# Performance work log

Hardware: AMD Instinct MI355X
Metric: run time of the kernel (lower is better)

## Reference

```python
import jax, jax.numpy as jnp
import numpy as np

B, V, FIN, H = 200, 40, 16, 128
NSW = 12          # switch edges
NE = 40           # regular edges
M = NE + NSW      # 52 total edges
MLP_HID = 1024
OUT = M + V + NSW # 104


def _build_graph():
    rng = np.random.default_rng(0)
    pairs = set()
    while len(pairs) < M:
        i, j = map(int, rng.integers(0, V, 2))
        if i < j:
            pairs.add((i, j))
    pairs = sorted(pairs)
    reg = np.array(pairs[:NE], np.int64)   # (NE,2)
    sw = np.array(pairs[NE:], np.int64)    # (NSW,2) row-major sorted, matches torch.nonzero order
    edges = np.concatenate([reg, sw], 0)   # switch edges last, matching graph_topo layout
    A = np.zeros((V, M), np.float32)
    A[edges[:, 0], np.arange(M)] = 1.0
    A[edges[:, 1], np.arange(M)] = -1.0
    return reg, sw, A


def setup_inputs():
    key = jax.random.key(0)
    ks = jax.random.split(key, 16)
    reg, sw, A = _build_graph()
    ei = jnp.broadcast_to(jnp.asarray(reg.T)[None], (B, 2, NE))
    si = jnp.broadcast_to(jnp.asarray(sw.T)[None], (B, 2, NSW))

    def w(k, shp, fan):
        return jax.random.normal(k, shp, jnp.float32) / np.sqrt(fan)

    return {
        'x_mod': jax.random.normal(ks[0], (B, V, FIN), jnp.float32),
        'ei': ei, 'si': si, 'A_inc': jnp.asarray(A),
        'embed': w(ks[1], (2, FIN), 1.0),
        'WU0': w(ks[2], (FIN, H), FIN), 'WV0': w(ks[3], (FIN, H), FIN),
        'WA0': w(ks[4], (FIN, H), FIN), 'WB0': w(ks[5], (FIN, H), FIN),
        'WC0': w(ks[6], (FIN, H), FIN),
        'WU1': w(ks[7], (H, H), H), 'WV1': w(ks[8], (H, H), H),
        'WA1': w(ks[9], (H, H), H), 'WB1': w(ks[10], (H, H), H),
        'WC1': w(ks[11], (H, H), H),
        'W1': w(ks[12], ((NSW + V) * H, MLP_HID), (NSW + V) * H),
        'b1': jnp.zeros((MLP_HID,), jnp.float32),
        'W2': w(ks[13], (MLP_HID, OUT), MLP_HID),
        'b2': jnp.zeros((OUT,), jnp.float32),
    }


def _layer(x, s, adj, smask, WU, WV, WA, WB, WC, residual):
    Ux = x @ WU
    Vx = x @ WV
    # gate features over dense VxV switch grid: e_ij = A s_ij + B x_i + C x_j
    e = jnp.einsum('bijf,fh->bijh', s, WA) + (x @ WB)[:, :, None, :] + (x @ WC)[:, None, :, :]
    gates = jax.nn.sigmoid(e) * smask[..., None]
    msg_edges = jnp.einsum('bij,bjh->bih', adj, Vx)   # regular-edge aggregation
    msg_sw = jnp.einsum('bijh,bjh->bih', gates, Vx)   # gated switch aggregation
    xh = jax.nn.relu(Ux + msg_edges + msg_sw)
    sh = jax.nn.relu(e)
    if residual:
        xh = x + xh
        sh = s + sh
    return xh, sh


def reference(x_mod, ei, si, A_inc, embed, WU0, WV0, WA0, WB0, WC0,
              WU1, WV1, WA1, WB1, WC1, W1, b1, W2, b2):
    i_sw, j_sw = si[0, 0], si[0, 1]   # switch indices (shared across batch)
    i_e, j_e = ei[0, 0], ei[0, 1]
    S = jnp.zeros((V, V), bool).at[i_sw, j_sw].set(True)   # upper-tri switch mask
    smask = jnp.broadcast_to(S, (B, V, V)).astype(x_mod.dtype)
    s0 = embed[S.astype(jnp.int32)]                        # (V,V,FIN) edge embedding
    s = jnp.broadcast_to(s0[None], (B, V, V, FIN))
    adj1 = jnp.zeros((V, V), x_mod.dtype).at[i_e, j_e].set(1.0)
    adj = jnp.broadcast_to((adj1 + adj1.T)[None], (B, V, V))
    x, s = _layer(x_mod, s, adj, smask, WU0, WV0, WA0, WB0, WC0, residual=False)
    x, s = _layer(x, s, adj, smask, WU1, WV1, WA1, WB1, WC1, residual=True)
    switches = s[:, i_sw, j_sw, :]                         # (B,NSW,H) irregular gather (torch.nonzero path)
    mlp_in = jnp.concatenate([switches.reshape(B, -1), x.reshape(B, -1)], axis=1)
    out = jax.nn.relu(mlp_in @ W1 + b1) @ W2 + b2          # (B,OUT)
    p_switch = jax.nn.sigmoid(out[:, -NSW:])
    graph_topo = jnp.ones((B, M), out.dtype).at[:, M - NSW:].set(p_switch)
    v = out[:, M:M + V].at[:, 0].set(1.0)
    p_fc = graph_topo * out[:, :M]
    q_fc = graph_topo * (v @ A_inc)                        # per-edge voltage difference flow
    pg = x_mod[:, :, 0] + jnp.einsum('vm,bm->bv', A_inc, p_fc)  # power balance completion
    qg = x_mod[:, :, 1] + jnp.einsum('vm,bm->bv', A_inc, q_fc)
    z = jnp.concatenate([p_fc, v, graph_topo], axis=1)     # (B, 2M+V)
    zc = jnp.concatenate([q_fc, pg, qg], axis=1)           # (B, M+2V)
    return z, zc
```

## Files before the change

### kernel.cpp

```cpp
#include <hip/hip_runtime.h>
#include <math.h>

#define B       200
#define V       40
#define FIN     16
#define H       128
#define NSW     12
#define NE      40
#define M       52
#define MLP_HID 1024
#define OUTD    104
#define MLP_IN  6656
#define ZDIM    144
#define ZCDIM   132
#define NCH     13
#define X1LD    136
#define MAXD    16

typedef __attribute__((ext_vector_type(8))) short bf16x8;
typedef __attribute__((ext_vector_type(4))) float f32x4;

__device__ __forceinline__ float sigmoidf(float x) {
    return 1.0f / (1.0f + expf(-x));
}
__device__ __forceinline__ unsigned short f2b(float x) {
    unsigned int u = __float_as_uint(x);
    u += 0x7fffu + ((u >> 16) & 1u);
    return (unsigned short)(u >> 16);
}
__device__ __forceinline__ float b2f(unsigned short s) {
    return __uint_as_float(((unsigned int)s) << 16);
}

__global__ __launch_bounds__(256) void k_prep(
        const float* __restrict__ WU0, const float* __restrict__ WV0,
        const float* __restrict__ WB0, const float* __restrict__ WC0,
        const float* __restrict__ WU1, const float* __restrict__ WV1,
        const float* __restrict__ WB1, const float* __restrict__ WC1,
        const float* __restrict__ WA1, const float* __restrict__ W2,
        unsigned short* __restrict__ W0t, unsigned short* __restrict__ Wt640,
        unsigned short* __restrict__ W2t) {
    int bx = blockIdx.x, tid = threadIdx.x;
    if (bx < 64) {
        int o0 = bx * 2048 + tid * 8;
#pragma unroll
        for (int i = 0; i < 8; ++i) {
            int o = o0 + i; int col = o >> 10, k = o & 1023;
            W2t[o] = (col < OUTD) ? f2b(W2[(size_t)k * OUTD + col]) : (unsigned short)0;
        }
    } else if (bx < 104) {
        int o0 = (bx - 64) * 2048 + tid * 8;
#pragma unroll
        for (int i = 0; i < 8; ++i) {
            int o = o0 + i; int col = o >> 7, f = o & 127;
            int m = col >> 7, hh = col & 127;
            const float* Ws = (m == 0) ? WU1 : (m == 1) ? WV1 : (m == 2) ? WB1
                            : (m == 3) ? WC1 : WA1;
            Wt640[o] = f2b(Ws[f * H + hh]);
        }
    } else {
        int o0 = (bx - 104) * 2048 + tid * 8;
#pragma unroll
        for (int i = 0; i < 8; ++i) {
            int o = o0 + i; int col = o >> 5, k = o & 31;
            int m = col >> 7, hh = col & 127;
            const float* Ws = (m == 0) ? WU0 : (m == 1) ? WV0 : (m == 2) ? WB0 : WC0;
            W0t[o] = (k < FIN) ? f2b(Ws[k * H + hh]) : (unsigned short)0;
        }
    }
}

__global__ __launch_bounds__(512) void k_gnn(const float* __restrict__ x,
        const int* __restrict__ ei, const int* __restrict__ si,
        const float* __restrict__ embed, const float* __restrict__ WA0,
        const unsigned short* __restrict__ W0t,
        const unsigned short* __restrict__ Wt640,
        unsigned short* __restrict__ Abf) {
    int b = blockIdx.x, tid = threadIdx.x;
    __shared__ unsigned short xb[48 * 40];
    __shared__ unsigned short uvbc[V * 512];
    __shared__ unsigned short x1l[64 * X1LD];
    __shared__ float gL[NSW * H];
    __shared__ float sA1l[NSW * H];
    __shared__ int   nbr[V][MAXD];
    __shared__ int   deg[V];

    int h = tid & 127, sub = tid >> 7;
    int lane = tid & 63, wv = tid >> 6;
    int lr = lane & 15, lk = lane >> 4;
    int n0w = wv * 64;

    for (int o = tid; o < 48 * 32; o += 512) {
        int r = o >> 5, k = o & 31;
        float v = (r < V && k < FIN) ? x[(size_t)b * V * FIN + r * FIN + k] : 0.f;
        xb[r * 40 + k] = f2b(v);
    }
    if (tid < V) deg[tid] = 0;
    for (int o = tid; o < 12 * 128; o += 512) {
        int rr = o >> 7;
        int row = (rr < 8) ? 40 + rr : 60 + (rr - 8);
        x1l[row * X1LD + (o & 127)] = 0;
    }
    __syncthreads();

    if (tid < NE) {
        int i = ei[tid], j = ei[NE + tid];
        int p = atomicAdd(&deg[i], 1); if (p < MAXD) nbr[i][p] = j;
        int q = atomicAdd(&deg[j], 1); if (q < MAXD) nbr[j][q] = i;
    } else if (tid < NE + NSW) {
        int k = tid - NE;
        int i = si[k], j = si[NSW + k];
        int p = atomicAdd(&deg[i], 1); if (p < MAXD) nbr[i][p] = j | ((k + 1) << 8);
    }
    {
        f32x4 acc[3][4];
#pragma unroll
        for (int rf = 0; rf < 3; ++rf)
#pragma unroll
            for (int cf = 0; cf < 4; ++cf) acc[rf][cf] = (f32x4){0.f, 0.f, 0.f, 0.f};
        int kseg = lk * 8;
        bf16x8 a0 = *(const bf16x8*)&xb[lr * 40 + kseg];
        bf16x8 a1 = *(const bf16x8*)&xb[(16 + lr) * 40 + kseg];
        bf16x8 a2 = *(const bf16x8*)&xb[(32 + lr) * 40 + kseg];
#pragma unroll
        for (int cf = 0; cf < 4; ++cf) {
            bf16x8 bf = *(const bf16x8*)&W0t[(n0w + cf * 16 + lr) * 32 + kseg];
            acc[0][cf] = __builtin_amdgcn_mfma_f32_16x16x32_bf16(a0, bf, acc[0][cf], 0, 0, 0);
            acc[1][cf] = __builtin_amdgcn_mfma_f32_16x16x32_bf16(a1, bf, acc[1][cf], 0, 0, 0);
            acc[2][cf] = __builtin_amdgcn_mfma_f32_16x16x32_bf16(a2, bf, acc[2][cf], 0, 0, 0);
        }
#pragma unroll
        for (int rf = 0; rf < 3; ++rf)
#pragma unroll
            for (int cf = 0; cf < 4; ++cf)
#pragma unroll
                for (int r = 0; r < 4; ++r) {
                    int row = rf * 16 + lk * 4 + r;
                    if (row < V) uvbc[row * 512 + n0w + cf * 16 + lr] = f2b(acc[rf][cf][r]);
                }
    }
    __syncthreads();

    {
        float sA0 = 0.f;
#pragma unroll
        for (int f = 0; f < FIN; ++f) sA0 += embed[FIN + f] * WA0[f * H + h];
        for (int k = sub; k < NSW; k += 4) {
            int i = si[k], j = si[NSW + k];
            float e0 = sA0 + b2f(uvbc[i * 512 + 256 + h]) + b2f(uvbc[j * 512 + 384 + h]);
            gL[k * H + h] = sigmoidf(e0);
            x1l[(48 + k) * X1LD + h] = f2b(fmaxf(e0, 0.f));
        }
    }
    __syncthreads();

    for (int i = sub * 10; i < sub * 10 + 10; ++i) {
        float acc = b2f(uvbc[i * 512 + h]);
        int d = deg[i]; if (d > MAXD) d = MAXD;
        for (int p = 0; p < d; ++p) {
            int ent = nbr[i][p];
            float vv = b2f(uvbc[(ent & 255) * 512 + 128 + h]);
            int g = ent >> 8;
            if (g) vv *= gL[(g - 1) * H + h];
            acc += vv;
        }
        x1l[i * X1LD + h] = f2b(fmaxf(acc, 0.f));
    }
    __syncthreads();

    {
        f32x4 acc[3][4], accs = (f32x4){0.f, 0.f, 0.f, 0.f};
#pragma unroll
        for (int rf = 0; rf < 3; ++rf)
#pragma unroll
            for (int cf = 0; cf < 4; ++cf) acc[rf][cf] = (f32x4){0.f, 0.f, 0.f, 0.f};
#pragma unroll
        for (int kk = 0; kk < 4; ++kk) {
            int kseg = kk * 32 + lk * 8;
            bf16x8 a0 = *(const bf16x8*)&x1l[lr * X1LD + kseg];
            bf16x8 a1 = *(const bf16x8*)&x1l[(16 + lr) * X1LD + kseg];
            bf16x8 a2 = *(const bf16x8*)&x1l[(32 + lr) * X1LD + kseg];
            bf16x8 as = *(const bf16x8*)&x1l[(48 + lr) * X1LD + kseg];
#pragma unroll
            for (int cf = 0; cf < 4; ++cf) {
                bf16x8 bf = *(const bf16x8*)&Wt640[(size_t)(n0w + cf * 16 + lr) * H + kseg];
                acc[0][cf] = __builtin_amdgcn_mfma_f32_16x16x32_bf16(a0, bf, acc[0][cf], 0, 0, 0);
                acc[1][cf] = __builtin_amdgcn_mfma_f32_16x16x32_bf16(a1, bf, acc[1][cf], 0, 0, 0);
                acc[2][cf] = __builtin_amdgcn_mfma_f32_16x16x32_bf16(a2, bf, acc[2][cf], 0, 0, 0);
            }
            bf16x8 bs = *(const bf16x8*)&Wt640[(size_t)(512 + wv * 16 + lr) * H + kseg];
            accs = __builtin_amdgcn_mfma_f32_16x16x32_bf16(as, bs, accs, 0, 0, 0);
        }
#pragma unroll
        for (int rf = 0; rf < 3; ++rf)
#pragma unroll
            for (int cf = 0; cf < 4; ++cf)
#pragma unroll
                for (int r = 0; r < 4; ++r) {
                    int row = rf * 16 + lk * 4 + r;
                    if (row < V) uvbc[row * 512 + n0w + cf * 16 + lr] = f2b(acc[rf][cf][r]);
                }
#pragma unroll
        for (int r = 0; r < 4; ++r) {
            int sr = lk * 4 + r;
            if (sr < NSW) sA1l[sr * H + wv * 16 + lr] = accs[r];
        }
    }
    __syncthreads();

    for (int k = sub; k < NSW; k += 4) {
        int i = si[k], j = si[NSW + k];
        float e1 = sA1l[k * H + h] + b2f(uvbc[i * 512 + 256 + h]) + b2f(uvbc[j * 512 + 384 + h]);
        gL[k * H + h] = sigmoidf(e1);
        float s1 = b2f(x1l[(48 + k) * X1LD + h]);
        Abf[(size_t)b * MLP_IN + k * H + h] = f2b(s1 + fmaxf(e1, 0.f));
    }
    __syncthreads();

    for (int i = sub * 10; i < sub * 10 + 10; ++i) {
        float acc = b2f(uvbc[i * 512 + h]);
        int d = deg[i]; if (d > MAXD) d = MAXD;
        for (int p = 0; p < d; ++p) {
            int ent = nbr[i][p];
            float vv = b2f(uvbc[(ent & 255) * 512 + 128 + h]);
            int g = ent >> 8;
            if (g) vv *= gL[(g - 1) * H + h];
            acc += vv;
        }
        float x2 = b2f(x1l[i * X1LD + h]) + fmaxf(acc, 0.f);
        Abf[(size_t)b * MLP_IN + NSW * H + i * H + h] = f2b(x2);
    }
}

__global__ __launch_bounds__(256) void k_mlp(const unsigned short* __restrict__ A,
        const float* __restrict__ W1, float* __restrict__ partial) {
    const int NK = 16;
    int tid = threadIdx.x;
    int lane = tid & 63, wvv = tid >> 6;
    int wr = (wvv >> 1) * 32, wc = (wvv & 1) * 32;
    int n0 = blockIdx.x * 64, m0 = blockIdx.y * 64;
    int kbase = blockIdx.z * NK * 32;

    __shared__ __align__(16) unsigned short a_lds[64 * 40];
    __shared__ __align__(16) unsigned short b_lds[64 * 40];

    f32x4 acc00 = {0,0,0,0}, acc01 = {0,0,0,0}, acc10 = {0,0,0,0}, acc11 = {0,0,0,0};

    int srow = tid >> 2, sseg = tid & 3;
    const int4* gA = (const int4*)(A + (size_t)(m0 + srow) * MLP_IN + kbase + sseg * 8);
    int lwsA = srow * 40 + sseg * 8;

    int bcol = tid & 63, bkg = tid >> 6;
    const float* gW = W1 + (size_t)(kbase + bkg * 8) * MLP_HID + n0 + bcol;
    int lwsB = bcol * 40 + bkg * 8;

    int a_off = (wr + (lane & 15)) * 40 + (lane >> 4) * 8;
    int b_off = (wc + (lane & 15)) * 40 + (lane >> 4) * 8;

    int4 ra = gA[0];
    float rfv[8];
#pragma unroll
    for (int i = 0; i < 8; ++i) rfv[i] = gW[(size_t)i * MLP_HID];

    for (int kk = 0; kk < NK; ++kk) {
        *(int4*)&a_lds[lwsA] = ra;
        union { unsigned short us[8]; int4 v; } pk;
#pragma unroll
        for (int i = 0; i < 8; ++i) pk.us[i] = f2b(rfv[i]);
        *(int4*)&b_lds[lwsB] = pk.v;
        __syncthreads();
        if (kk + 1 < NK) {
            ra = gA[(kk + 1) * 4];
            const float* g2 = gW + (size_t)(kk + 1) * 32 * MLP_HID;
#pragma unroll
            for (int i = 0; i < 8; ++i) rfv[i] = g2[(size_t)i * MLP_HID];
        }
        bf16x8 a0 = *(const bf16x8*)&a_lds[a_off];
        bf16x8 a1 = *(const bf16x8*)&a_lds[a_off + 16 * 40];
        bf16x8 b0 = *(const bf16x8*)&b_lds[b_off];
        bf16x8 b1 = *(const bf16x8*)&b_lds[b_off + 16 * 40];
        acc00 = __builtin_amdgcn_mfma_f32_16x16x32_bf16(a0, b0, acc00, 0, 0, 0);
        acc01 = __builtin_amdgcn_mfma_f32_16x16x32_bf16(a0, b1, acc01, 0, 0, 0);
        acc10 = __builtin_amdgcn_mfma_f32_16x16x32_bf16(a1, b0, acc10, 0, 0, 0);
        acc11 = __builtin_amdgcn_mfma_f32_16x16x32_bf16(a1, b1, acc11, 0, 0, 0);
        __syncthreads();
    }

    int crow = (lane >> 4) * 4, ccol = lane & 15;
    int row0 = m0 + wr + crow, row1 = row0 + 16;
    int col0 = n0 + wc + ccol, col1 = col0 + 16;
    float* dst = partial + (size_t)blockIdx.z * 256 * MLP_HID;
#pragma unroll
    for (int r = 0; r < 4; ++r) {
        dst[(size_t)(row0 + r) * MLP_HID + col0] = acc00[r];
        dst[(size_t)(row0 + r) * MLP_HID + col1] = acc01[r];
        dst[(size_t)(row1 + r) * MLP_HID + col0] = acc10[r];
        dst[(size_t)(row1 + r) * MLP_HID + col1] = acc11[r];
    }
}

template<int MODE>
__global__ __launch_bounds__(256) void k_gemm(const unsigned short* __restrict__ A,
        const unsigned short* __restrict__ Bt, void* __restrict__ Cout,
        int K, int nk, int ldc) {
    int tid = threadIdx.x;
    int lane = tid & 63, wv = tid >> 6;
    int wr = (wv >> 1) * 32, wc = (wv & 1) * 32;
    int n0 = blockIdx.x * 64, m0 = blockIdx.y * 64;
    size_t kbase = (size_t)blockIdx.z * nk * 32;

    __shared__ __align__(16) unsigned short a_lds[64 * 40];
    __shared__ __align__(16) unsigned short b_lds[64 * 40];

    f32x4 acc00 = {0,0,0,0}, acc01 = {0,0,0,0}, acc10 = {0,0,0,0}, acc11 = {0,0,0,0};

    int srow = tid >> 2, sseg = tid & 3;
    const int4* gA = (const int4*)(A + (size_t)(m0 + srow) * K + kbase + sseg * 8);
    const int4* gB = (const int4*)(Bt + (size_t)(n0 + srow) * K + kbase + sseg * 8);
    int lws = srow * 40 + sseg * 8;

    int a_off = (wr + (lane & 15)) * 40 + (lane >> 4) * 8;
    int b_off = (wc + (lane & 15)) * 40 + (lane >> 4) * 8;

    int4 ra = gA[0], rb = gB[0];
    for (int kk = 0; kk < nk; ++kk) {
        *(int4*)&a_lds[lws] = ra;
        *(int4*)&b_lds[lws] = rb;
        __syncthreads();
        if (kk + 1 < nk) { ra = gA[(kk + 1) * 4]; rb = gB[(kk + 1) * 4]; }
        bf16x8 a0 = *(const bf16x8*)&a_lds[a_off];
        bf16x8 a1 = *(const bf16x8*)&a_lds[a_off + 16 * 40];
        bf16x8 b0 = *(const bf16x8*)&b_lds[b_off];
        bf16x8 b1 = *(const bf16x8*)&b_lds[b_off + 16 * 40];
        acc00 = __builtin_amdgcn_mfma_f32_16x16x32_bf16(a0, b0, acc00, 0, 0, 0);
        acc01 = __builtin_amdgcn_mfma_f32_16x16x32_bf16(a0, b1, acc01, 0, 0, 0);
        acc10 = __builtin_amdgcn_mfma_f32_16x16x32_bf16(a1, b0, acc10, 0, 0, 0);
        acc11 = __builtin_amdgcn_mfma_f32_16x16x32_bf16(a1, b1, acc11, 0, 0, 0);
        __syncthreads();
    }

    int crow = (lane >> 4) * 4, ccol = lane & 15;
    int row0 = m0 + wr + crow, row1 = row0 + 16;
    int col0 = n0 + wc + ccol, col1 = col0 + 16;
    float* dst = (float*)Cout + (size_t)blockIdx.z * (gridDim.y * 64) * ldc;
#pragma unroll
    for (int r = 0; r < 4; ++r) {
        dst[(size_t)(row0 + r) * ldc + col0] = acc00[r];
        dst[(size_t)(row0 + r) * ldc + col1] = acc01[r];
        dst[(size_t)(row1 + r) * ldc + col0] = acc10[r];
        dst[(size_t)(row1 + r) * ldc + col1] = acc11[r];
    }
}

__global__ void k_mred(const float* __restrict__ partial, const float* __restrict__ b1,
                       unsigned short* __restrict__ hiddenb) {
    int i = blockIdx.x * 256 + threadIdx.x;
    float s = b1[i & (MLP_HID - 1)];
#pragma unroll
    for (int z = 0; z < NCH; ++z) s += partial[(size_t)z * 256 * MLP_HID + i];
    hiddenb[i] = f2b(fmaxf(s, 0.f));
}

__global__ __launch_bounds__(128) void k_fin(const float* __restrict__ partial2,
        const float* __restrict__ b2, const float* __restrict__ A,
        const float* __restrict__ x_mod, float* __restrict__ outp) {
    int b = blockIdx.x;
    int tid = threadIdx.x;
    __shared__ float o[OUTD];
    __shared__ float gt[M], vv[V], pfc[M], qfc[M];

    if (tid < OUTD) {
        float s = b2[tid];
#pragma unroll
        for (int z = 0; z < 4; ++z) s += partial2[(size_t)z * 256 * 128 + b * 128 + tid];
        o[tid] = s;
    }
    __syncthreads();

    if (tid < M) {
        float g = (tid < M - NSW) ? 1.0f : sigmoidf(o[M + V + (tid - (M - NSW))]);
        gt[tid] = g;
        pfc[tid] = g * o[tid];
    }
    if (tid < V) vv[tid] = (tid == 0) ? 1.0f : o[M + tid];
    __syncthreads();

    if (tid < M) {
        float acc = 0.f;
        for (int x = 0; x < V; ++x) acc += vv[x] * A[x * M + tid];
        qfc[tid] = gt[tid] * acc;
    }
    __syncthreads();

    float* zb = outp + (size_t)b * ZDIM;
    if (tid < M) zb[tid] = pfc[tid];
    if (tid < V) zb[M + tid] = vv[tid];
    if (tid < M) zb[M + V + tid] = gt[tid];

    float* zcb = outp + (size_t)B * ZDIM + (size_t)b * ZCDIM;
    if (tid < M) zcb[tid] = qfc[tid];
    if (tid < V) {
        float accp = 0.f, accq = 0.f;
        for (int m = 0; m < M; ++m) {
            float a = A[tid * M + m];
            accp += a * pfc[m];
            accq += a * qfc[m];
        }
        zcb[M + tid]     = x_mod[(size_t)(b * V + tid) * FIN + 0] + accp;
        zcb[M + V + tid] = x_mod[(size_t)(b * V + tid) * FIN + 1] + accq;
    }
}

extern "C" void kernel_launch(void* const* d_in, const int* in_sizes, int n_in,
                              void* d_out, int out_size, void* d_ws, size_t ws_size,
                              hipStream_t stream) {
    const float* x_mod = (const float*)d_in[0];
    const int*   ei    = (const int*)d_in[1];
    const int*   si    = (const int*)d_in[2];
    const float* A     = (const float*)d_in[3];
    const float* embed = (const float*)d_in[4];
    const float* WU0   = (const float*)d_in[5];
    const float* WV0   = (const float*)d_in[6];
    const float* WA0   = (const float*)d_in[7];
    const float* WB0   = (const float*)d_in[8];
    const float* WC0   = (const float*)d_in[9];
    const float* WU1   = (const float*)d_in[10];
    const float* WV1   = (const float*)d_in[11];
    const float* WA1   = (const float*)d_in[12];
    const float* WB1   = (const float*)d_in[13];
    const float* WC1   = (const float*)d_in[14];
    const float* W1    = (const float*)d_in[15];
    const float* b1    = (const float*)d_in[16];
    const float* W2    = (const float*)d_in[17];
    const float* b2    = (const float*)d_in[18];
    float* out = (float*)d_out;

    char* ws = (char*)d_ws;
    unsigned short* W0t      = (unsigned short*)(ws + 0);
    unsigned short* Wt640    = (unsigned short*)(ws + 32768);
    unsigned short* W2t      = (unsigned short*)(ws + 196608);
    unsigned short* Abf      = (unsigned short*)(ws + 458752);
    float*          partialM = (float*)(ws + 3866624);
    unsigned short* hiddenb  = (unsigned short*)(ws + 17498112);
    float*          partial2 = (float*)(ws + 18022400);

    k_prep<<<112, 256, 0, stream>>>(WU0, WV0, WB0, WC0, WU1, WV1, WB1, WC1, WA1, W2,
                                    W0t, Wt640, W2t);
    k_gnn<<<B, 512, 0, stream>>>(x_mod, ei, si, embed, WA0, W0t, Wt640, Abf);
    k_mlp<<<dim3(16, 4, NCH), 256, 0, stream>>>(Abf, W1, partialM);
    k_mred<<<256 * MLP_HID / 256, 256, 0, stream>>>(partialM, b1, hiddenb);
    k_gemm<2><<<dim3(2, 4, 4), 256, 0, stream>>>(hiddenb, W2t, partial2, MLP_HID, 8, 128);
    k_fin<<<B, 128, 0, stream>>>(partial2, b2, A, x_mod, out);
}
```

Measured before the change: 56.48 us.

## Fuse all stages into one cooperative persistent kernel with grid syncs

Replaces six separate kernel launches (weight prep, GNN, MLP split-K, reduction, second GEMM, finalize) with a single cooperative kernel of 256 blocks. Stages are separated by grid-wide syncs and share one LDS union. The aim is to remove per-launch overhead and inter-kernel gaps. In exchange, the stages now run at a fixed grid size with larger blocks, grid.sync has its own cost, and occupancy is constrained by the cooperative launch.

```diff
diff --git a/kernel.cpp b/kernel.cpp
--- a/kernel.cpp
+++ b/kernel.cpp
@@ -1,5 +1,8 @@
 #include <hip/hip_runtime.h>
+#include <hip/hip_cooperative_groups.h>
 #include <math.h>
+
+namespace cg = cooperative_groups;
 
 #define B       200
 #define V       40
@@ -32,382 +35,401 @@
     return __uint_as_float(((unsigned int)s) << 16);
 }
 
-__global__ __launch_bounds__(256) void k_prep(
+__global__ __launch_bounds__(512, 2) void k_all(
+        const float* __restrict__ x_mod, const int* __restrict__ ei,
+        const int* __restrict__ si, const float* __restrict__ Ainc,
+        const float* __restrict__ embed,
         const float* __restrict__ WU0, const float* __restrict__ WV0,
-        const float* __restrict__ WB0, const float* __restrict__ WC0,
+        const float* __restrict__ WA0, const float* __restrict__ WB0,
+        const float* __restrict__ WC0,
         const float* __restrict__ WU1, const float* __restrict__ WV1,
-        const float* __restrict__ WB1, const float* __restrict__ WC1,
-        const float* __restrict__ WA1, const float* __restrict__ W2,
+        const float* __restrict__ WA1, const float* __restrict__ WB1,
+        const float* __restrict__ WC1,
+        const float* __restrict__ W1, const float* __restrict__ b1,
+        const float* __restrict__ W2, const float* __restrict__ b2,
         unsigned short* __restrict__ W0t, unsigned short* __restrict__ Wt640,
-        unsigned short* __restrict__ W2t) {
-    int bx = blockIdx.x, tid = threadIdx.x;
-    if (bx < 64) {
-        int o0 = bx * 2048 + tid * 8;
-#pragma unroll
-        for (int i = 0; i < 8; ++i) {
-            int o = o0 + i; int col = o >> 10, k = o & 1023;
+        unsigned short* __restrict__ W2t, unsigned short* __restrict__ Abf,
+        float* __restrict__ partialM, unsigned short* __restrict__ hiddenb,
+        float* __restrict__ partial2, float* __restrict__ outp) {
+    cg::grid_group grid = cg::this_grid();
+    int bid = blockIdx.x, tid = threadIdx.x;
+    int gtid = bid * 512 + tid;
+
+    __shared__ union {
+        struct {
+            unsigned short xb[48 * 40];
+            unsigned short uvbc[V * 512];
+            unsigned short x1l[64 * X1LD];
+            float gL[NSW * H];
+            float sA1l[NSW * H];
+            int   nbr[V][MAXD];
+            int   deg[V];
+        } g;
+        struct { unsigned short a[64 * 40]; unsigned short b[128 * 40]; } m;
+        struct { float o[OUTD]; float gt[M]; float vv[V]; float pfc[M]; float qfc[M]; } f;
+    } lds;
+
+    for (int t = gtid; t < 16384 + 81920 + 131072; t += 131072) {
+        if (t < 16384) {
+            int col = t >> 5, k = t & 31;
+            int mm = col >> 7, hh = col & 127;
+            const float* Ws = (mm == 0) ? WU0 : (mm == 1) ? WV0 : (mm == 2) ? WB0 : WC0;
+            W0t[t] = (k < FIN) ? f2b(Ws[k * H + hh]) : (unsigned short)0;
+        } else if (t < 16384 + 81920) {
+            int o = t - 16384;
+            int col = o >> 7, ff = o & 127;
+            int mm = col >> 7, hh = col & 127;
+            const float* Ws = (mm == 0) ? WU1 : (mm == 1) ? WV1 : (mm == 2) ? WB1
+                            : (mm == 3) ? WC1 : WA1;
+            Wt640[o] = f2b(Ws[ff * H + hh]);
+        } else {
+            int o = t - (16384 + 81920);
+            int col = o >> 10, k = o & 1023;
             W2t[o] = (col < OUTD) ? f2b(W2[(size_t)k * OUTD + col]) : (unsigned short)0;
         }
-    } else if (bx < 104) {
-        int o0 = (bx - 64) * 2048 + tid * 8;
-#pragma unroll
-        for (int i = 0; i < 8; ++i) {
-            int o = o0 + i; int col = o >> 7, f = o & 127;
-            int m = col >> 7, hh = col & 127;
-            const float* Ws = (m == 0) ? WU1 : (m == 1) ? WV1 : (m == 2) ? WB1
-                            : (m == 3) ? WC1 : WA1;
-            Wt640[o] = f2b(Ws[f * H + hh]);
-        }
-    } else {
-        int o0 = (bx - 104) * 2048 + tid * 8;
-#pragma unroll
-        for (int i = 0; i < 8; ++i) {
-            int o = o0 + i; int col = o >> 5, k = o & 31;
-            int m = col >> 7, hh = col & 127;
-            const float* Ws = (m == 0) ? WU0 : (m == 1) ? WV0 : (m == 2) ? WB0 : WC0;
-            W0t[o] = (k < FIN) ? f2b(Ws[k * H + hh]) : (unsigned short)0;
-        }
-    }
-}
-
-__global__ __launch_bounds__(512) void k_gnn(const float* __restrict__ x,
-        const int* __restrict__ ei, const int* __restrict__ si,
-        const float* __restrict__ embed, const float* __restrict__ WA0,
-        const unsigned short* __restrict__ W0t,
-        const unsigned short* __restrict__ Wt640,
-        unsigned short* __restrict__ Abf) {
-    int b = blockIdx.x, tid = threadIdx.x;
-    __shared__ unsigned short xb[48 * 40];
-    __shared__ unsigned short uvbc[V * 512];
-    __shared__ unsigned short x1l[64 * X1LD];
-    __shared__ float gL[NSW * H];
-    __shared__ float sA1l[NSW * H];
-    __shared__ int   nbr[V][MAXD];
-    __shared__ int   deg[V];
-
-    int h = tid & 127, sub = tid >> 7;
-    int lane = tid & 63, wv = tid >> 6;
-    int lr = lane & 15, lk = lane >> 4;
-    int n0w = wv * 64;
-
-    for (int o = tid; o < 48 * 32; o += 512) {
-        int r = o >> 5, k = o & 31;
-        float v = (r < V && k < FIN) ? x[(size_t)b * V * FIN + r * FIN + k] : 0.f;
-        xb[r * 40 + k] = f2b(v);
-    }
-    if (tid < V) deg[tid] = 0;
-    for (int o = tid; o < 12 * 128; o += 512) {
-        int rr = o >> 7;
-        int row = (rr < 8) ? 40 + rr : 60 + (rr - 8);
-        x1l[row * X1LD + (o & 127)] = 0;
-    }
-    __syncthreads();
-
-    if (tid < NE) {
-        int i = ei[tid], j = ei[NE + tid];
-        int p = atomicAdd(&deg[i], 1); if (p < MAXD) nbr[i][p] = j;
-        int q = atomicAdd(&deg[j], 1); if (q < MAXD) nbr[j][q] = i;
-    } else if (tid < NE + NSW) {
-        int k = tid - NE;
-        int i = si[k], j = si[NSW + k];
-        int p = atomicAdd(&deg[i], 1); if (p < MAXD) nbr[i][p] = j | ((k + 1) << 8);
-    }
-    {
-        f32x4 acc[3][4];
-#pragma unroll
-        for (int rf = 0; rf < 3; ++rf)
-#pragma unroll
-            for (int cf = 0; cf < 4; ++cf) acc[rf][cf] = (f32x4){0.f, 0.f, 0.f, 0.f};
-        int kseg = lk * 8;
-        bf16x8 a0 = *(const bf16x8*)&xb[lr * 40 + kseg];
-        bf16x8 a1 = *(const bf16x8*)&xb[(16 + lr) * 40 + kseg];
-        bf16x8 a2 = *(const bf16x8*)&xb[(32 + lr) * 40 + kseg];
-#pragma unroll
-        for (int cf = 0; cf < 4; ++cf) {
-            bf16x8 bf = *(const bf16x8*)&W0t[(n0w + cf * 16 + lr) * 32 + kseg];
-            acc[0][cf] = __builtin_amdgcn_mfma_f32_16x16x32_bf16(a0, bf, acc[0][cf], 0, 0, 0);
-            acc[1][cf] = __builtin_amdgcn_mfma_f32_16x16x32_bf16(a1, bf, acc[1][cf], 0, 0, 0);
-            acc[2][cf] = __builtin_amdgcn_mfma_f32_16x16x32_bf16(a2, bf, acc[2][cf], 0, 0, 0);
-        }
-#pragma unroll
-        for (int rf = 0; rf < 3; ++rf)
-#pragma unroll
-            for (int cf = 0; cf < 4; ++cf)
-#pragma unroll
-                for (int r = 0; r < 4; ++r) {
-                    int row = rf * 16 + lk * 4 + r;
-                    if (row < V) uvbc[row * 512 + n0w + cf * 16 + lr] = f2b(acc[rf][cf][r]);
-                }
-    }
-    __syncthreads();
-
-    {
-        float sA0 = 0.f;
-#pragma unroll
-        for (int f = 0; f < FIN; ++f) sA0 += embed[FIN + f] * WA0[f * H + h];
-        for (int k = sub; k < NSW; k += 4) {
+    }
+    grid.sync();
+
+    if (bid < B) {
+        int b = bid;
+        unsigned short* xb   = lds.g.xb;
+        unsigned short* uvbc = lds.g.uvbc;
+        unsigned short* x1l  = lds.g.x1l;
+        float* gL   = lds.g.gL;
+        float* sA1l = lds.g.sA1l;
+        int (*nbr)[MAXD] = lds.g.nbr;
+        int* deg = lds.g.deg;
+
+        int h = tid & 127, sub = tid >> 7;
+        int lane = tid & 63, wv = tid >> 6;
+        int lr = lane & 15, lk = lane >> 4;
+        int n0w = wv * 64;
+
+        for (int o = tid; o < 48 * 32; o += 512) {
+            int r = o >> 5, k = o & 31;
+            float v = (r < V && k < FIN) ? x_mod[(size_t)b * V * FIN + r * FIN + k] : 0.f;
+            xb[r * 40 + k] = f2b(v);
+        }
+        if (tid < V) deg[tid] = 0;
+        for (int o = tid; o < 12 * 128; o += 512) {
+            int rr = o >> 7;
+            int row = (rr < 8) ? 40 + rr : 60 + (rr - 8);
+            x1l[row * X1LD + (o & 127)] = 0;
+        }
+        __syncthreads();
+
+        if (tid < NE) {
+            int i = ei[tid], j = ei[NE + tid];
+            int p = atomicAdd(&deg[i], 1); if (p < MAXD) nbr[i][p] = j;
+            int q = atomicAdd(&deg[j], 1); if (q < MAXD) nbr[j][q] = i;
+        } else if (tid < NE + NSW) {
+            int k = tid - NE;
             int i = si[k], j = si[NSW + k];
-            float e0 = sA0 + b2f(uvbc[i * 512 + 256 + h]) + b2f(uvbc[j * 512 + 384 + h]);
-            gL[k * H + h] = sigmoidf(e0);
-            x1l[(48 + k) * X1LD + h] = f2b(fmaxf(e0, 0.f));
-        }
-    }
-    __syncthreads();
-
-    for (int i = sub * 10; i < sub * 10 + 10; ++i) {
-        float acc = b2f(uvbc[i * 512 + h]);
-        int d = deg[i]; if (d > MAXD) d = MAXD;
-        for (int p = 0; p < d; ++p) {
-            int ent = nbr[i][p];
-            float vv = b2f(uvbc[(ent & 255) * 512 + 128 + h]);
-            int g = ent >> 8;
-            if (g) vv *= gL[(g - 1) * H + h];
-            acc += vv;
-        }
-        x1l[i * X1LD + h] = f2b(fmaxf(acc, 0.f));
-    }
-    __syncthreads();
-
-    {
-        f32x4 acc[3][4], accs = (f32x4){0.f, 0.f, 0.f, 0.f};
-#pragma unroll
-        for (int rf = 0; rf < 3; ++rf)
-#pragma unroll
-            for (int cf = 0; cf < 4; ++cf) acc[rf][cf] = (f32x4){0.f, 0.f, 0.f, 0.f};
-#pragma unroll
-        for (int kk = 0; kk < 4; ++kk) {
-            int kseg = kk * 32 + lk * 8;
-            bf16x8 a0 = *(const bf16x8*)&x1l[lr * X1LD + kseg];
-            bf16x8 a1 = *(const bf16x8*)&x1l[(16 + lr) * X1LD + kseg];
-            bf16x8 a2 = *(const bf16x8*)&x1l[(32 + lr) * X1LD + kseg];
-            bf16x8 as = *(const bf16x8*)&x1l[(48 + lr) * X1LD + kseg];
+            int p = atomicAdd(&deg[i], 1); if (p < MAXD) nbr[i][p] = j | ((k + 1) << 8);
+        }
+        {
+            f32x4 acc[3][4];
+#pragma unroll
+            for (int rf = 0; rf < 3; ++rf)
+#pragma unroll
+                for (int cf = 0; cf < 4; ++cf) acc[rf][cf] = (f32x4){0.f, 0.f, 0.f, 0.f};
+            int kseg = lk * 8;
+            bf16x8 a0 = *(const bf16x8*)&xb[lr * 40 + kseg];
+            bf16x8 a1 = *(const bf16x8*)&xb[(16 + lr) * 40 + kseg];
+            bf16x8 a2 = *(const bf16x8*)&xb[(32 + lr) * 40 + kseg];
 #pragma unroll
             for (int cf = 0; cf < 4; ++cf) {
-                bf16x8 bf = *(const bf16x8*)&Wt640[(size_t)(n0w + cf * 16 + lr) * H + kseg];
+                bf16x8 bf = *(const bf16x8*)&W0t[(n0w + cf * 16 + lr) * 32 + kseg];
                 acc[0][cf] = __builtin_amdgcn_mfma_f32_16x16x32_bf16(a0, bf, acc[0][cf], 0, 0, 0);
                 acc[1][cf] = __builtin_amdgcn_mfma_f32_16x16x32_bf16(a1, bf, acc[1][cf], 0, 0, 0);
                 acc[2][cf] = __builtin_amdgcn_mfma_f32_16x16x32_bf16(a2, bf, acc[2][cf], 0, 0, 0);
             }
-            bf16x8 bs = *(const bf16x8*)&Wt640[(size_t)(512 + wv * 16 + lr) * H + kseg];
-            accs = __builtin_amdgcn_mfma_f32_16x16x32_bf16(as, bs, accs, 0, 0, 0);
-        }
-#pragma unroll
-        for (int rf = 0; rf < 3; ++rf)
-#pragma unroll
-            for (int cf = 0; cf < 4; ++cf)
+#pragma unroll
+            for (int rf = 0; rf < 3; ++rf)
+#pragma unroll
+                for (int cf = 0; cf < 4; ++cf)
+#pragma unroll
+                    for (int r = 0; r < 4; ++r) {
+                        int row = rf * 16 + lk * 4 + r;
+                        if (row < V) uvbc[row * 512 + n0w + cf * 16 + lr] = f2b(acc[rf][cf][r]);
+                    }
+        }
+        __syncthreads();
+
+        {
+            float sA0 = 0.f;
+#pragma unroll
+            for (int f = 0; f < FIN; ++f) sA0 += embed[FIN + f] * WA0[f * H + h];
+            for (int k = sub; k < NSW; k += 4) {
+                int i = si[k], j = si[NSW + k];
+                float e0 = sA0 + b2f(uvbc[i * 512 + 256 + h]) + b2f(uvbc[j * 512 + 384 + h]);
+                gL[k * H + h] = sigmoidf(e0);
+                x1l[(48 + k) * X1LD + h] = f2b(fmaxf(e0, 0.f));
+            }
+        }
+        __syncthreads();
+
+        for (int i = sub * 10; i < sub * 10 + 10; ++i) {
+            float acc = b2f(uvbc[i * 512 + h]);
+            int d = deg[i]; if (d > MAXD) d = MAXD;
+            for (int p = 0; p < d; ++p) {
+                int ent = nbr[i][p];
+                float vv = b2f(uvbc[(ent & 255) * 512 + 128 + h]);
+                int g = ent >> 8;
+                if (g) vv *= gL[(g - 1) * H + h];
+                acc += vv;
+            }
+            x1l[i * X1LD + h] = f2b(fmaxf(acc, 0.f));
+        }
+        __syncthreads();
+
+        {
+            f32x4 acc[3][4], accs = (f32x4){0.f, 0.f, 0.f, 0.f};
+#pragma unroll
+            for (int rf = 0; rf < 3; ++rf)
+#pragma unroll
+                for (int cf = 0; cf < 4; ++cf) acc[rf][cf] = (f32x4){0.f, 0.f, 0.f, 0.f};
+#pragma unroll
+            for (int kk = 0; kk < 4; ++kk) {
+                int kseg = kk * 32 + lk * 8;
+                bf16x8 a0 = *(const bf16x8*)&x1l[lr * X1LD + kseg];
+                bf16x8 a1 = *(const bf16x8*)&x1l[(16 + lr) * X1LD + kseg];
+                bf16x8 a2 = *(const bf16x8*)&x1l[(32 + lr) * X1LD + kseg];
+                bf16x8 as = *(const bf16x8*)&x1l[(48 + lr) * X1LD + kseg];
+#pragma unroll
+                for (int cf = 0; cf < 4; ++cf) {
+                    bf16x8 bf = *(const bf16x8*)&Wt640[(size_t)(n0w + cf * 16 + lr) * H + kseg];
+                    acc[0][cf] = __builtin_amdgcn_mfma_f32_16x16x32_bf16(a0, bf, acc[0][cf], 0, 0, 0);
+                    acc[1][cf] = __builtin_amdgcn_mfma_f32_16x16x32_bf16(a1, bf, acc[1][cf], 0, 0, 0);
+                    acc[2][cf] = __builtin_amdgcn_mfma_f32_16x16x32_bf16(a2, bf, acc[2][cf], 0, 0, 0);
+                }
+                bf16x8 bs = *(const bf16x8*)&Wt640[(size_t)(512 + wv * 16 + lr) * H + kseg];
+                accs = __builtin_amdgcn_mfma_f32_16x16x32_bf16(as, bs, accs, 0, 0, 0);
+            }
+#pragma unroll
+            for (int rf = 0; rf < 3; ++rf)
+#pragma unroll
+                for (int cf = 0; cf < 4; ++cf)
+#pragma unroll
+                    for (int r = 0; r < 4; ++r) {
+                        int row = rf * 16 + lk * 4 + r;
+                        if (row < V) uvbc[row * 512 + n0w + cf * 16 + lr] = f2b(acc[rf][cf][r]);
+                    }
+#pragma unroll
+            for (int r = 0; r < 4; ++r) {
+                int sr = lk * 4 + r;
+                if (sr < NSW) sA1l[sr * H + wv * 16 + lr] = accs[r];
+            }
+        }
+        __syncthreads();
+
+        for (int k = sub; k < NSW; k += 4) {
+            int i = si[k], j = si[NSW + k];
+            float e1 = sA1l[k * H + h] + b2f(uvbc[i * 512 + 256 + h]) + b2f(uvbc[j * 512 + 384 + h]);
+            gL[k * H + h] = sigmoidf(e1);
+            float s1 = b2f(x1l[(48 + k) * X1LD + h]);
+            Abf[(size_t)b * MLP_IN + k * H + h] = f2b(s1 + fmaxf(e1, 0.f));
+        }
+        __syncthreads();
+
+        for (int i = sub * 10; i < sub * 10 + 10; ++i) {
+            float acc = b2f(uvbc[i * 512 + h]);
+            int d = deg[i]; if (d > MAXD) d = MAXD;
+            for (int p = 0; p < d; ++p) {
+                int ent = nbr[i][p];
+                float vv = b2f(uvbc[(ent & 255) * 512 + 128 + h]);
+                int g = ent >> 8;
+                if (g) vv *= gL[(g - 1) * H + h];
+                acc += vv;
+            }
+            float x2 = b2f(x1l[i * X1LD + h]) + fmaxf(acc, 0.f);
+            Abf[(size_t)b * MLP_IN + NSW * H + i * H + h] = f2b(x2);
+        }
+    }
+    grid.sync();
+
+    {
+        unsigned short* a_lds = lds.m.a;
+        unsigned short* b_lds = lds.m.b;
+        int lane = tid & 63, wv = tid >> 6;
+        int lr = lane & 15, lk = lane >> 4;
+        int wr = (wv >> 2) * 32, wc = (wv & 3) * 32;
+
+        for (int it = 0; it < 2; ++it) {
+            int j = bid + it * 256;
+            bool valid = (j < 416);
+            int jj = valid ? j : 0;
+            int z = jj >> 5;
+            int rem = jj & 31;
+            int n0 = (rem & 7) << 7;
+            int m0 = (rem >> 3) << 6;
+            int kbase = z << 9;
+
+            int srow = tid >> 3, sseg = tid & 7;
+            const unsigned short* gA = Abf + (size_t)(m0 + srow) * MLP_IN + kbase + sseg * 4;
+            int lwsA = srow * 40 + sseg * 4;
+            int bcol = tid & 127, bkg = tid >> 7;
+            const float* gW = W1 + (size_t)(kbase + bkg * 8) * MLP_HID + n0 + bcol;
+            int lwsB = bcol * 40 + bkg * 8;
+            int a_off = (wr + lr) * 40 + lk * 8;
+            int b_off = (wc + lr) * 40 + lk * 8;
+
+            f32x4 acc00 = {0,0,0,0}, acc01 = {0,0,0,0}, acc10 = {0,0,0,0}, acc11 = {0,0,0,0};
+            int2 ra = *(const int2*)gA;
+            float rfv[8];
+#pragma unroll
+            for (int i = 0; i < 8; ++i) rfv[i] = gW[(size_t)i * MLP_HID];
+
+            for (int kk = 0; kk < 16; ++kk) {
+                *(int2*)&a_lds[lwsA] = ra;
+                union { unsigned short us[8]; int4 v; } pk;
+#pragma unroll
+                for (int i = 0; i < 8; ++i) pk.us[i] = f2b(rfv[i]);
+                *(int4*)&b_lds[lwsB] = pk.v;
+                __syncthreads();
+                if (kk + 1 < 16) {
+                    ra = *(const int2*)(gA + (kk + 1) * 32);
+                    const float* g2 = gW + (size_t)(kk + 1) * 32 * MLP_HID;
+#pragma unroll
+                    for (int i = 0; i < 8; ++i) rfv[i] = g2[(size_t)i * MLP_HID];
+                }
+                bf16x8 a0 = *(const bf16x8*)&a_lds[a_off];
+                bf16x8 a1 = *(const bf16x8*)&a_lds[a_off + 16 * 40];
+                bf16x8 b0 = *(const bf16x8*)&b_lds[b_off];
+                bf16x8 b1 = *(const bf16x8*)&b_lds[b_off + 16 * 40];
+                acc00 = __builtin_amdgcn_mfma_f32_16x16x32_bf16(a0, b0, acc00, 0, 0, 0);
+                acc01 = __builtin_amdgcn_mfma_f32_16x16x32_bf16(a0, b1, acc01, 0, 0, 0);
+                acc10 = __builtin_amdgcn_mfma_f32_16x16x32_bf16(a1, b0, acc10, 0, 0, 0);
+                acc11 = __builtin_amdgcn_mfma_f32_16x16x32_bf16(a1, b1, acc11, 0, 0, 0);
+                __syncthreads();
+            }
+            if (valid) {
+                int crow = lk * 4, ccol = lr;
+                int row0 = m0 + wr + crow, row1 = row0 + 16;
+                int col0 = n0 + wc + ccol, col1 = col0 + 16;
+                float* dst = partialM + (size_t)z * 256 * MLP_HID;
 #pragma unroll
                 for (int r = 0; r < 4; ++r) {
-                    int row = rf * 16 + lk * 4 + r;
-                    if (row < V) uvbc[row * 512 + n0w + cf * 16 + lr] = f2b(acc[rf][cf][r]);
+                    dst[(size_t)(row0 + r) * MLP_HID + col0] = acc00[r];
+                    dst[(size_t)(row0 + r) * MLP_HID + col1] = acc01[r];
+                    dst[(size_t)(row1 + r) * MLP_HID + col0] = acc10[r];
+                    dst[(size_t)(row1 + r) * MLP_HID + col1] = acc11[r];
                 }
+            }
+        }
+    }
+    grid.sync();
+
+    for (int t = gtid; t < 256 * MLP_HID; t += 131072) {
+        float s = b1[t & (MLP_HID - 1)];
+#pragma unroll
+        for (int z = 0; z < NCH; ++z) s += partialM[(size_t)z * 256 * MLP_HID + t];
+        hiddenb[t] = f2b(fmaxf(s, 0.f));
+    }
+    grid.sync();
+
+    if (bid < 16) {
+        unsigned short* a_lds = lds.m.a;
+        unsigned short* b_lds = lds.m.b;
+        int m0 = (bid >> 2) * 64;
+        int z = bid & 3;
+        int kbase = z * 256;
+        int lane = tid & 63, wv = tid >> 6;
+        int lr = lane & 15, lk = lane >> 4;
+        int wr = (wv >> 2) * 32, wc = (wv & 3) * 32;
+
+        int srow = tid >> 3, sseg = tid & 7;
+        const unsigned short* gA = hiddenb + (size_t)(m0 + srow) * MLP_HID + kbase + sseg * 4;
+        int lwsA = srow * 40 + sseg * 4;
+        int brow = tid >> 2, bseg = tid & 3;
+        const unsigned short* gB = W2t + (size_t)brow * MLP_HID + kbase + bseg * 8;
+        int lwsB = brow * 40 + bseg * 8;
+        int a_off = (wr + lr) * 40 + lk * 8;
+        int b_off = (wc + lr) * 40 + lk * 8;
+
+        f32x4 acc00 = {0,0,0,0}, acc01 = {0,0,0,0}, acc10 = {0,0,0,0}, acc11 = {0,0,0,0};
+        int2 ra = *(const int2*)gA;
+        int4 rb = *(const int4*)gB;
+        for (int kk = 0; kk < 8; ++kk) {
+            *(int2*)&a_lds[lwsA] = ra;
+            *(int4*)&b_lds[lwsB] = rb;
+            __syncthreads();
+            if (kk + 1 < 8) {
+                ra = *(const int2*)(gA + (kk + 1) * 32);
+                rb = *(const int4*)(gB + (kk + 1) * 32);
+            }
+            bf16x8 a0 = *(const bf16x8*)&a_lds[a_off];
+            bf16x8 a1 = *(const bf16x8*)&a_lds[a_off + 16 * 40];
+            bf16x8 b0 = *(const bf16x8*)&b_lds[b_off];
+            bf16x8 b1 = *(const bf16x8*)&b_lds[b_off + 16 * 40];
+            acc00 = __builtin_amdgcn_mfma_f32_16x16x32_bf16(a0, b0, acc00, 0, 0, 0);
+            acc01 = __builtin_amdgcn_mfma_f32_16x16x32_bf16(a0, b1, acc01, 0, 0, 0);
+            acc10 = __builtin_amdgcn_mfma_f32_16x16x32_bf16(a1, b0, acc10, 0, 0, 0);
+            acc11 = __builtin_amdgcn_mfma_f32_16x16x32_bf16(a1, b1, acc11, 0, 0, 0);
+            __syncthreads();
+        }
+        int crow = lk * 4, ccol = lr;
+        int row0 = m0 + wr + crow, row1 = row0 + 16;
+        int col0 = wc + ccol, col1 = col0 + 16;
+        float* dst = partial2 + (size_t)z * 256 * 128;
 #pragma unroll
         for (int r = 0; r < 4; ++r) {
-            int sr = lk * 4 + r;
-            if (sr < NSW) sA1l[sr * H + wv * 16 + lr] = accs[r];
-        }
-    }
-    __syncthreads();
-
-    for (int k = sub; k < NSW; k += 4) {
-        int i = si[k], j = si[NSW + k];
-        float e1 = sA1l[k * H + h] + b2f(uvbc[i * 512 + 256 + h]) + b2f(uvbc[j * 512 + 384 + h]);
-        gL[k * H + h] = sigmoidf(e1);
-        float s1 = b2f(x1l[(48 + k) * X1LD + h]);
-        Abf[(size_t)b * MLP_IN + k * H + h] = f2b(s1 + fmaxf(e1, 0.f));
-    }
-    __syncthreads();
-
-    for (int i = sub * 10; i < sub * 10 + 10; ++i) {
-        float acc = b2f(uvbc[i * 512 + h]);
-        int d = deg[i]; if (d > MAXD) d = MAXD;
-        for (int p = 0; p < d; ++p) {
-            int ent = nbr[i][p];
-            float vv = b2f(uvbc[(ent & 255) * 512 + 128 + h]);
-            int g = ent >> 8;
-            if (g) vv *= gL[(g - 1) * H + h];
-            acc += vv;
-        }
-        float x2 = b2f(x1l[i * X1LD + h]) + fmaxf(acc, 0.f);
-        Abf[(size_t)b * MLP_IN + NSW * H + i * H + h] = f2b(x2);
-    }
-}
-
-__global__ __launch_bounds__(256) void k_mlp(const unsigned short* __restrict__ A,
-        const float* __restrict__ W1, float* __restrict__ partial) {
-    const int NK = 16;
-    int tid = threadIdx.x;
-    int lane = tid & 63, wvv = tid >> 6;
-    int wr = (wvv >> 1) * 32, wc = (wvv & 1) * 32;
-    int n0 = blockIdx.x * 64, m0 = blockIdx.y * 64;
-    int kbase = blockIdx.z * NK * 32;
-
-    __shared__ __align__(16) unsigned short a_lds[64 * 40];
-    __shared__ __align__(16) unsigned short b_lds[64 * 40];
-
-    f32x4 acc00 = {0,0,0,0}, acc01 = {0,0,0,0}, acc10 = {0,0,0,0}, acc11 = {0,0,0,0};
-
-    int srow = tid >> 2, sseg = tid & 3;
-    const int4* gA = (const int4*)(A + (size_t)(m0 + srow) * MLP_IN + kbase + sseg * 8);
-    int lwsA = srow * 40 + sseg * 8;
-
-    int bcol = tid & 63, bkg = tid >> 6;
-    const float* gW = W1 + (size_t)(kbase + bkg * 8) * MLP_HID + n0 + bcol;
-    int lwsB = bcol * 40 + bkg * 8;
-
-    int a_off = (wr + (lane & 15)) * 40 + (lane >> 4) * 8;
-    int b_off = (wc + (lane & 15)) * 40 + (lane >> 4) * 8;
-
-    int4 ra = gA[0];
-    float rfv[8];
-#pragma unroll
-    for (int i = 0; i < 8; ++i) rfv[i] = gW[(size_t)i * MLP_HID];
-
-    for (int kk = 0; kk < NK; ++kk) {
-        *(int4*)&a_lds[lwsA] = ra;
-        union { unsigned short us[8]; int4 v; } pk;
-#pragma unroll
-        for (int i = 0; i < 8; ++i) pk.us[i] = f2b(rfv[i]);
-        *(int4*)&b_lds[lwsB] = pk.v;
-        __syncthreads();
-        if (kk + 1 < NK) {
-            ra = gA[(kk + 1) * 4];
-            const float* g2 = gW + (size_t)(kk + 1) * 32 * MLP_HID;
-#pragma unroll
-            for (int i = 0; i < 8; ++i) rfv[i] = g2[(size_t)i * MLP_HID];
-        }
-        bf16x8 a0 = *(const bf16x8*)&a_lds[a_off];
-        bf16x8 a1 = *(const bf16x8*)&a_lds[a_off + 16 * 40];
-        bf16x8 b0 = *(const bf16x8*)&b_lds[b_off];
-        bf16x8 b1 = *(const bf16x8*)&b_lds[b_off + 16 * 40];
-        acc00 = __builtin_amdgcn_mfma_f32_16x16x32_bf16(a0, b0, acc00, 0, 0, 0);
-        acc01 = __builtin_amdgcn_mfma_f32_16x16x32_bf16(a0, b1, acc01, 0, 0, 0);
-        acc10 = __builtin_amdgcn_mfma_f32_16x16x32_bf16(a1, b0, acc10, 0, 0, 0);
-        acc11 = __builtin_amdgcn_mfma_f32_16x16x32_bf16(a1, b1, acc11, 0, 0, 0);
-        __syncthreads();
-    }
-
-    int crow = (lane >> 4) * 4, ccol = lane & 15;
-    int row0 = m0 + wr + crow, row1 = row0 + 16;
-    int col0 = n0 + wc + ccol, col1 = col0 + 16;
-    float* dst = partial + (size_t)blockIdx.z * 256 * MLP_HID;
-#pragma unroll
-    for (int r = 0; r < 4; ++r) {
-        dst[(size_t)(row0 + r) * MLP_HID + col0] = acc00[r];
-        dst[(size_t)(row0 + r) * MLP_HID + col1] = acc01[r];
-        dst[(size_t)(row1 + r) * MLP_HID + col0] = acc10[r];
-        dst[(size_t)(row1 + r) * MLP_HID + col1] = acc11[r];
-    }
-}
-
-template<int MODE>
-__global__ __launch_bounds__(256) void k_gemm(const unsigned short* __restrict__ A,
-        const unsigned short* __restrict__ Bt, void* __restrict__ Cout,
-        int K, int nk, int ldc) {
-    int tid = threadIdx.x;
-    int lane = tid & 63, wv = tid >> 6;
-    int wr = (wv >> 1) * 32, wc = (wv & 1) * 32;
-    int n0 = blockIdx.x * 64, m0 = blockIdx.y * 64;
-    size_t kbase = (size_t)blockIdx.z * nk * 32;
-
-    __shared__ __align__(16) unsigned short a_lds[64 * 40];
-    __shared__ __align__(16) unsigned short b_lds[64 * 40];
-
-    f32x4 acc00 = {0,0,0,0}, acc01 = {0,0,0,0}, acc10 = {0,0,0,0}, acc11 = {0,0,0,0};
-
-    int srow = tid >> 2, sseg = tid & 3;
-    const int4* gA = (const int4*)(A + (size_t)(m0 + srow) * K + kbase + sseg * 8);
-    const int4* gB = (const int4*)(Bt + (size_t)(n0 + srow) * K + kbase + sseg * 8);
-    int lws = srow * 40 + sseg * 8;
-
-    int a_off = (wr + (lane & 15)) * 40 + (lane >> 4) * 8;
-    int b_off = (wc + (lane & 15)) * 40 + (lane >> 4) * 8;
-
-    int4 ra = gA[0], rb = gB[0];
-    for (int kk = 0; kk < nk; ++kk) {
-        *(int4*)&a_lds[lws] = ra;
-        *(int4*)&b_lds[lws] = rb;
-        __syncthreads();
-        if (kk + 1 < nk) { ra = gA[(kk + 1) * 4]; rb = gB[(kk + 1) * 4]; }
-        bf16x8 a0 = *(const bf16x8*)&a_lds[a_off];
-        bf16x8 a1 = *(const bf16x8*)&a_lds[a_off + 16 * 40];
-        bf16x8 b0 = *(const bf16x8*)&b_lds[b_off];
-        bf16x8 b1 = *(const bf16x8*)&b_lds[b_off + 16 * 40];
-        acc00 = __builtin_amdgcn_mfma_f32_16x16x32_bf16(a0, b0, acc00, 0, 0, 0);
-        acc01 = __builtin_amdgcn_mfma_f32_16x16x32_bf16(a0, b1, acc01, 0, 0, 0);
-        acc10 = __builtin_amdgcn_mfma_f32_16x16x32_bf16(a1, b0, acc10, 0, 0, 0);
-        acc11 = __builtin_amdgcn_mfma_f32_16x16x32_bf16(a1, b1, acc11, 0, 0, 0);
-        __syncthreads();
-    }
-
-    int crow = (lane >> 4) * 4, ccol = lane & 15;
-    int row0 = m0 + wr + crow, row1 = row0 + 16;
-    int col0 = n0 + wc + ccol, col1 = col0 + 16;
-    float* dst = (float*)Cout + (size_t)blockIdx.z * (gridDim.y * 64) * ldc;
-#pragma unroll
-    for (int r = 0; r < 4; ++r) {
-        dst[(size_t)(row0 + r) * ldc + col0] = acc00[r];
-        dst[(size_t)(row0 + r) * ldc + col1] = acc01[r];
-        dst[(size_t)(row1 + r) * ldc + col0] = acc10[r];
-        dst[(size_t)(row1 + r) * ldc + col1] = acc11[r];
-    }
-}
-
-__global__ void k_mred(const float* __restrict__ partial, const float* __restrict__ b1,
-                       unsigned short* __restrict__ hiddenb) {
-    int i = blockIdx.x * 256 + threadIdx.x;
-    float s = b1[i & (MLP_HID - 1)];
-#pragma unroll
-    for (int z = 0; z < NCH; ++z) s += partial[(size_t)z * 256 * MLP_HID + i];
-    hiddenb[i] = f2b(fmaxf(s, 0.f));
-}
-
-__global__ __launch_bounds__(128) void k_fin(const float* __restrict__ partial2,
-        const float* __restrict__ b2, const float* __restrict__ A,
-        const float* __restrict__ x_mod, float* __restrict__ outp) {
-    int b = blockIdx.x;
-    int tid = threadIdx.x;
-    __shared__ float o[OUTD];
-    __shared__ float gt[M], vv[V], pfc[M], qfc[M];
-
-    if (tid < OUTD) {
-        float s = b2[tid];
-#pragma unroll
-        for (int z = 0; z < 4; ++z) s += partial2[(size_t)z * 256 * 128 + b * 128 + tid];
-        o[tid] = s;
-    }
-    __syncthreads();
-
-    if (tid < M) {
-        float g = (tid < M - NSW) ? 1.0f : sigmoidf(o[M + V + (tid - (M - NSW))]);
-        gt[tid] = g;
-        pfc[tid] = g * o[tid];
-    }
-    if (tid < V) vv[tid] = (tid == 0) ? 1.0f : o[M + tid];
-    __syncthreads();
-
-    if (tid < M) {
-        float acc = 0.f;
-        for (int x = 0; x < V; ++x) acc += vv[x] * A[x * M + tid];
-        qfc[tid] = gt[tid] * acc;
-    }
-    __syncthreads();
-
-    float* zb = outp + (size_t)b * ZDIM;
-    if (tid < M) zb[tid] = pfc[tid];
-    if (tid < V) zb[M + tid] = vv[tid];
-    if (tid < M) zb[M + V + tid] = gt[tid];
-
-    float* zcb = outp + (size_t)B * ZDIM + (size_t)b * ZCDIM;
-    if (tid < M) zcb[tid] = qfc[tid];
-    if (tid < V) {
-        float accp = 0.f, accq = 0.f;
-        for (int m = 0; m < M; ++m) {
-            float a = A[tid * M + m];
-            accp += a * pfc[m];
-            accq += a * qfc[m];
-        }
-        zcb[M + tid]     = x_mod[(size_t)(b * V + tid) * FIN + 0] + accp;
-        zcb[M + V + tid] = x_mod[(size_t)(b * V + tid) * FIN + 1] + accq;
+            dst[(size_t)(row0 + r) * 128 + col0] = acc00[r];
+            dst[(size_t)(row0 + r) * 128 + col1] = acc01[r];
+            dst[(size_t)(row1 + r) * 128 + col0] = acc10[r];
+            dst[(size_t)(row1 + r) * 128 + col1] = acc11[r];
+        }
+    }
+    grid.sync();
+
+    if (bid < B) {
+        int b = bid;
+        float* o   = lds.f.o;
+        float* gt  = lds.f.gt;
+        float* vv  = lds.f.vv;
+        float* pfc = lds.f.pfc;
+        float* qfc = lds.f.qfc;
+
+        if (tid < OUTD) {
+            float s = b2[tid];
+#pragma unroll
+            for (int z = 0; z < 4; ++z) s += partial2[(size_t)z * 256 * 128 + b * 128 + tid];
+            o[tid] = s;
+        }
+        __syncthreads();
+
+        if (tid < M) {
+            float g = (tid < M - NSW) ? 1.0f : sigmoidf(o[M + V + (tid - (M - NSW))]);
+            gt[tid] = g;
+            pfc[tid] = g * o[tid];
+        }
+        if (tid < V) vv[tid] = (tid == 0) ? 1.0f : o[M + tid];
+        __syncthreads();
+
+        if (tid < M) {
+            float acc = 0.f;
+            for (int xx = 0; xx < V; ++xx) acc += vv[xx] * Ainc[xx * M + tid];
+            qfc[tid] = gt[tid] * acc;
+        }
+        __syncthreads();
+
+        float* zb = outp + (size_t)b * ZDIM;
+        if (tid < M) zb[tid] = pfc[tid];
+        if (tid < V) zb[M + tid] = vv[tid];
+        if (tid < M) zb[M + V + tid] = gt[tid];
+
+        float* zcb = outp + (size_t)B * ZDIM + (size_t)b * ZCDIM;
+        if (tid < M) zcb[tid] = qfc[tid];
+        if (tid < V) {
+            float accp = 0.f, accq = 0.f;
+            for (int mm = 0; mm < M; ++mm) {
+                float a = Ainc[tid * M + mm];
+                accp += a * pfc[mm];
+                accq += a * qfc[mm];
+            }
+            zcb[M + tid]     = x_mod[(size_t)(b * V + tid) * FIN + 0] + accp;
+            zcb[M + V + tid] = x_mod[(size_t)(b * V + tid) * FIN + 1] + accq;
+        }
     }
 }
 
@@ -417,7 +439,7 @@
     const float* x_mod = (const float*)d_in[0];
     const int*   ei    = (const int*)d_in[1];
     const int*   si    = (const int*)d_in[2];
-    const float* A     = (const float*)d_in[3];
+    const float* Ainc  = (const float*)d_in[3];
     const float* embed = (const float*)d_in[4];
     const float* WU0   = (const float*)d_in[5];
     const float* WV0   = (const float*)d_in[6];
@@ -444,11 +466,14 @@
     unsigned short* hiddenb  = (unsigned short*)(ws + 17498112);
     float*          partial2 = (float*)(ws + 18022400);
 
-    k_prep<<<112, 256, 0, stream>>>(WU0, WV0, WB0, WC0, WU1, WV1, WB1, WC1, WA1, W2,
-                                    W0t, Wt640, W2t);
-    k_gnn<<<B, 512, 0, stream>>>(x_mod, ei, si, embed, WA0, W0t, Wt640, Abf);
-    k_mlp<<<dim3(16, 4, NCH), 256, 0, stream>>>(Abf, W1, partialM);
-    k_mred<<<256 * MLP_HID / 256, 256, 0, stream>>>(partialM, b1, hiddenb);
-    k_gemm<2><<<dim3(2, 4, 4), 256, 0, stream>>>(hiddenb, W2t, partial2, MLP_HID, 8, 128);
-    k_fin<<<B, 128, 0, stream>>>(partial2, b2, A, x_mod, out);
+    void* kargs[] = {
+        (void*)&x_mod, (void*)&ei, (void*)&si, (void*)&Ainc, (void*)&embed,
+        (void*)&WU0, (void*)&WV0, (void*)&WA0, (void*)&WB0, (void*)&WC0,
+        (void*)&WU1, (void*)&WV1, (void*)&WA1, (void*)&WB1, (void*)&WC1,
+        (void*)&W1, (void*)&b1, (void*)&W2, (void*)&b2,
+        (void*)&W0t, (void*)&Wt640, (void*)&W2t, (void*)&Abf,
+        (void*)&partialM, (void*)&hiddenb, (void*)&partial2, (void*)&out
+    };
+    hipLaunchCooperativeKernel((const void*)k_all, dim3(256), dim3(512),
+                               kargs, 0, stream);
 }
```

Measured after the change: 209.6 us. +271.1%, slower.
